# Kernel tuning notes

Hardware: AMD Instinct MI355X
Metric: run time of the kernel (lower is better)

Reference implementation:

```python
import jax, jax.numpy as jnp
import numpy as np

# Config (matches init_kwargs)
S = 8            # num_seqs
LQ = 256         # query tokens per sequence (num_tokens = S*LQ = 2048)
SEQ = 2048       # kv seq_len per sequence
BLK = 16         # block size
NBLK_PER_SEQ = SEQ // BLK   # 128 = max_num_blocks_per_seq
NUM_BLKS = S * NBLK_PER_SEQ # 1024
HQ = 32          # num_query_heads
HKV = 8          # num_kv_heads
G = HQ // HKV    # queries per kv head (GQA group)
D = 128          # head_size
WINDOW = 1024    # sliding_window
SCALE = 1.0 / float(np.sqrt(D))


def setup_inputs() -> dict:
    key = jax.random.key(0)
    k1, k2, k3 = jax.random.split(key, 3)
    query = jax.random.normal(k1, (S * LQ, HQ, D), jnp.float32)
    key_cache = jax.random.normal(k2, (NUM_BLKS, BLK, HKV, D), jnp.float32)
    value_cache = jax.random.normal(k3, (NUM_BLKS, BLK, HKV, D), jnp.float32)
    # each sequence owns a contiguous run of blocks; all indices valid (>=0)
    block_tables = jnp.arange(NUM_BLKS, dtype=jnp.int32).reshape(S, NBLK_PER_SEQ)
    seq_lens = jnp.full((S,), SEQ, dtype=jnp.int32)
    query_start_len = (jnp.arange(S + 1, dtype=jnp.int32) * LQ)
    return dict(query=query, key_cache=key_cache, value_cache=value_cache,
                block_tables=block_tables, seq_lens=seq_lens,
                query_start_len=query_start_len)


def reference(query, key_cache, value_cache, block_tables, seq_lens, query_start_len):
    # query: [S*LQ, HQ, D] -> [S, LQ, HKV, G, D]
    q = query.reshape(S, LQ, HKV, G, D)
    # paged KV gather: [S, NBLK_PER_SEQ] -> [S, NBLK_PER_SEQ, BLK, HKV, D] -> [S, SEQ, HKV, D]
    K = key_cache[block_tables].reshape(S, SEQ, HKV, D)
    V = value_cache[block_tables].reshape(S, SEQ, HKV, D)
    # attention scores: [S, HKV, G, LQ, SEQ]
    scores = jnp.einsum('sqhgd,skhd->shgqk', q, K) * SCALE
    # causal + sliding-window mask over absolute positions
    ctx = SEQ - LQ  # context_len (same for all seqs here)
    qpos = ctx + jnp.arange(LQ)          # [LQ] absolute query positions
    kpos = jnp.arange(SEQ)               # [SEQ] absolute key positions
    valid = (kpos[None, :] <= qpos[:, None]) & \
            (qpos[:, None] - kpos[None, :] < WINDOW)   # [LQ, SEQ]
    neg_inf = jnp.asarray(-jnp.inf, scores.dtype)
    scores = jnp.where(valid[None, None, None, :, :], scores, neg_inf)
    probs = jax.nn.softmax(scores, axis=-1)
    # output: [S, LQ, HKV, G, D] -> [S*LQ, HQ, D]
    out = jnp.einsum('shgqk,skhd->sqhgd', probs, V)
    return out.reshape(S * LQ, HQ, D)
```

## Files before the change

kernel.cpp:

```cpp
#include <hip/hip_runtime.h>
#include <stdint.h>

typedef __attribute__((ext_vector_type(8))) short short8;
typedef __attribute__((ext_vector_type(4))) float floatx4;
typedef __attribute__((ext_vector_type(16))) float f32x16;
typedef __attribute__((ext_vector_type(4))) unsigned int uint4v;
typedef __attribute__((ext_vector_type(2))) unsigned int uint2v;

#define NSEQ 8
#define BLKSZ 16
#define NBLK_PER_SEQ 128
#define HQN 32
#define HKVN 8
#define GQ 4
#define HD 128
#define WINDOW 1024
#define QSCALE 0.12751744f

#define QB 32
#define KVB 64
#define KROW 136
#define VROW 72

#define MFMA32 __builtin_amdgcn_mfma_f32_32x32x16_bf16

static __device__ __forceinline__ unsigned int pack2bf(float lo, float hi) {
    unsigned int a = __builtin_bit_cast(unsigned int, lo) + 0x8000u;
    unsigned int b = __builtin_bit_cast(unsigned int, hi) + 0x8000u;
    return __builtin_amdgcn_perm(b, a, 0x07060302u);
}

static __device__ __forceinline__ float xhalf_max(float x) {
    return fmaxf(x, __shfl_xor(x, 32));
}

extern __shared__ char smem[];

__global__ __launch_bounds__(256, 2)
void attn_fwd(const float* __restrict__ qg,
              const float* __restrict__ kg,
              const float* __restrict__ vg,
              const int* __restrict__ bt,
              const int* __restrict__ seqlens,
              const int* __restrict__ qsl,
              float* __restrict__ outg)
{
    short (*Klds)[KVB][KROW] = (short(*)[KVB][KROW])smem;
    short (*Vt)[HD][VROW]    = (short(*)[HD][VROW])(smem + 34816);

    const int tid  = threadIdx.x;
    const int lane = tid & 63;
    const int wave = tid >> 6;
    const int l31  = lane & 31;
    const int hi   = lane >> 5;

    const int b  = blockIdx.x;
    const int h  = b & 7;
    const int qt = (b >> 3) & 7;
    const int s  = b >> 6;
    const int q0 = qt * QB;

    const int qstart = qsl[s];
    const int numq   = qsl[s + 1] - qstart;
    const int slen   = seqlens[s];
    const int ctx    = slen - numq;
    const int hq     = h * GQ + wave;

    short8 qf[8];
    {
        const float* qrow = qg + ((size_t)(qstart + q0 + l31) * HQN + hq) * HD;
        #pragma unroll
        for (int ks = 0; ks < 8; ++ks) {
            floatx4 f0 = *(const floatx4*)(qrow + ks * 16 + hi * 8);
            floatx4 f1 = *(const floatx4*)(qrow + ks * 16 + hi * 8 + 4);
            uint4v w;
            w[0] = pack2bf(f0[0] * QSCALE, f0[1] * QSCALE);
            w[1] = pack2bf(f0[2] * QSCALE, f0[3] * QSCALE);
            w[2] = pack2bf(f1[0] * QSCALE, f1[1] * QSCALE);
            w[3] = pack2bf(f1[2] * QSCALE, f1[3] * QSCALE);
            qf[ks] = __builtin_bit_cast(short8, w);
        }
    }

    f32x16 oacc[4];
    #pragma unroll
    for (int dblk = 0; dblk < 4; ++dblk)
        #pragma unroll
        for (int i = 0; i < 16; ++i)
            oacc[dblk][i] = 0.f;

    float mrun = -INFINITY;
    float lrun = 0.f;

    int lo = ctx + q0 - WINDOW + 1; if (lo < 0) lo = 0;
    int hiq = ctx + q0 + QB - 1;    if (hiq > slen - 1) hiq = slen - 1;
    const int t0 = lo / KVB, t1 = hiq / KVB;

    const int srow = tid >> 3;
    const int sd0  = (tid & 7) * 16;
    const int j4   = tid & 15;
    const int d0v  = (tid >> 4) * 8;

    floatx4 fk[8], fv[8];

#define LOAD_K_HALF(kv0_, p) {                                                       \
        const int kvp = (kv0_) + (p) * 32 + srow;                                    \
        const int blk = bt[s * NBLK_PER_SEQ + (kvp >> 4)];                           \
        const float* src = kg + (((size_t)blk * BLKSZ + (kvp & 15)) * HKVN + h) * HD + sd0; \
        fk[(p)*4+0] = *(const floatx4*)(src);                                        \
        fk[(p)*4+1] = *(const floatx4*)(src + 4);                                    \
        fk[(p)*4+2] = *(const floatx4*)(src + 8);                                    \
        fk[(p)*4+3] = *(const floatx4*)(src + 12);                                   \
    }
#define LOAD_V(kv0_) {                                                               \
        const int kvv = (kv0_) + 4 * j4;                                             \
        const int blkv = bt[s * NBLK_PER_SEQ + (kvv >> 4)];                          \
        const float* vsrc = vg + (((size_t)blkv * BLKSZ + (kvv & 15)) * HKVN + h) * HD + d0v; \
        fv[0] = *(const floatx4*)(vsrc);                                             \
        fv[4] = *(const floatx4*)(vsrc + 4);                                         \
        fv[1] = *(const floatx4*)(vsrc + 1024);                                      \
        fv[5] = *(const floatx4*)(vsrc + 1028);                                      \
        fv[2] = *(const floatx4*)(vsrc + 2048);                                      \
        fv[6] = *(const floatx4*)(vsrc + 2052);                                      \
        fv[3] = *(const floatx4*)(vsrc + 3072);                                      \
        fv[7] = *(const floatx4*)(vsrc + 3076);                                      \
    }
#define LOAD_TILE(kv0_) { LOAD_K_HALF(kv0_, 0); LOAD_K_HALF(kv0_, 1); LOAD_V(kv0_); }

    LOAD_TILE(t0 * KVB);

    for (int t = t0; t <= t1; ++t) {
        const int kv0 = t * KVB;
        const int vb  = t & 1;

        #pragma unroll
        for (int p = 0; p < 2; ++p) {
            const int row = p * 32 + srow;
            uint4v w;
            w[0] = pack2bf(fk[p*4+0][0], fk[p*4+0][1]);
            w[1] = pack2bf(fk[p*4+0][2], fk[p*4+0][3]);
            w[2] = pack2bf(fk[p*4+1][0], fk[p*4+1][1]);
            w[3] = pack2bf(fk[p*4+1][2], fk[p*4+1][3]);
            *(uint4v*)&Klds[vb][row][sd0] = w;
            w[0] = pack2bf(fk[p*4+2][0], fk[p*4+2][1]);
            w[1] = pack2bf(fk[p*4+2][2], fk[p*4+2][3]);
            w[2] = pack2bf(fk[p*4+3][0], fk[p*4+3][1]);
            w[3] = pack2bf(fk[p*4+3][2], fk[p*4+3][3]);
            *(uint4v*)&Klds[vb][row][sd0 + 8] = w;
        }
        #pragma unroll
        for (int d = 0; d < 8; ++d) {
            const float r0 = (d < 4) ? fv[0][d] : fv[4][d - 4];
            const float r1 = (d < 4) ? fv[1][d] : fv[5][d - 4];
            const float r2 = (d < 4) ? fv[2][d] : fv[6][d - 4];
            const float r3 = (d < 4) ? fv[3][d] : fv[7][d - 4];
            uint2v w;
            w[0] = pack2bf(r0, r1);
            w[1] = pack2bf(r2, r3);
            *(uint2v*)&Vt[vb][d0v + d][4 * j4] = w;
        }

        __syncthreads();

        f32x16 sacc0, sacc1;
        #pragma unroll
        for (int i = 0; i < 16; ++i) { sacc0[i] = 0.f; sacc1[i] = 0.f; }
        #pragma unroll
        for (int ks = 0; ks < 8; ++ks) {
            short8 kf0 = *(const short8*)&Klds[vb][l31][ks * 16 + hi * 8];
            short8 kf1 = *(const short8*)&Klds[vb][32 + l31][ks * 16 + hi * 8];
            sacc0 = MFMA32(kf0, qf[ks], sacc0, 0, 0, 0);
            sacc1 = MFMA32(kf1, qf[ks], sacc1, 0, 0, 0);
        }

        if (t < t1) LOAD_TILE(kv0 + KVB);

        const bool interior = (kv0 >= ctx + q0 - (WINDOW - QB)) &&
                              (kv0 + KVB - 1 <= ctx + q0);
        const int qpos = ctx + q0 + l31;
        float p2[2][16];
        #pragma unroll
        for (int m2 = 0; m2 < 2; ++m2) {
            #pragma unroll
            for (int r = 0; r < 16; ++r) {
                float x = (m2 == 0) ? sacc0[r] : sacc1[r];
                if (!interior) {
                    const int kpos = kv0 + m2 * 32 + (r & 3) + 4 * hi + 8 * (r >> 2);
                    const bool valid = (kpos <= qpos) && (qpos - kpos < WINDOW);
                    x = valid ? x : -INFINITY;
                }
                p2[m2][r] = x;
            }
        }
        float tmax[16];
        #pragma unroll
        for (int r = 0; r < 16; ++r) tmax[r] = fmaxf(p2[0][r], p2[1][r]);
        #pragma unroll
        for (int s2 = 8; s2 > 0; s2 >>= 1)
            #pragma unroll
            for (int r = 0; r < 8; ++r)
                if (r < s2) tmax[r] = fmaxf(tmax[r], tmax[r + s2]);
        float rmax = xhalf_max(tmax[0]);

        const float mold = mrun;
        const bool defer = __all(rmax <= mold + 11.0f);
        const float mnew = defer ? mold : fmaxf(mold, rmax);
        const float alpha = defer ? 1.0f
            : ((mold == -INFINITY) ? ((mnew == -INFINITY) ? 1.0f : 0.0f)
                                   : exp2f(mold - mnew));
        const bool dead = (mnew == -INFINITY);
        #pragma unroll
        for (int m2 = 0; m2 < 2; ++m2)
            #pragma unroll
            for (int r = 0; r < 16; ++r)
                p2[m2][r] = dead ? 0.f : exp2f(p2[m2][r] - mnew);
        float ts[16];
        #pragma unroll
        for (int r = 0; r < 16; ++r) ts[r] = p2[0][r] + p2[1][r];
        #pragma unroll
        for (int s2 = 8; s2 > 0; s2 >>= 1)
            #pragma unroll
            for (int r = 0; r < 8; ++r)
                if (r < s2) ts[r] = ts[r] + ts[r + s2];
        lrun = lrun * alpha + ts[0];
        mrun = mnew;
        if (!defer) {
            #pragma unroll
            for (int dblk = 0; dblk < 4; ++dblk)
                oacc[dblk] = oacc[dblk] * alpha;
        }

        short8 pb[2][2];
        #pragma unroll
        for (int m2 = 0; m2 < 2; ++m2) {
            unsigned int c0 = pack2bf(p2[m2][0],  p2[m2][1]);
            unsigned int c1 = pack2bf(p2[m2][2],  p2[m2][3]);
            unsigned int c2 = pack2bf(p2[m2][4],  p2[m2][5]);
            unsigned int c3 = pack2bf(p2[m2][6],  p2[m2][7]);
            unsigned int c4 = pack2bf(p2[m2][8],  p2[m2][9]);
            unsigned int c5 = pack2bf(p2[m2][10], p2[m2][11]);
            unsigned int c6 = pack2bf(p2[m2][12], p2[m2][13]);
            unsigned int c7 = pack2bf(p2[m2][14], p2[m2][15]);
            unsigned int s0 = hi ? c0 : c2;
            unsigned int s1 = hi ? c1 : c3;
            unsigned int s2 = hi ? c4 : c6;
            unsigned int s3 = hi ? c5 : c7;
            unsigned int r0 = (unsigned int)__shfl_xor((int)s0, 32);
            unsigned int r1 = (unsigned int)__shfl_xor((int)s1, 32);
            unsigned int r2 = (unsigned int)__shfl_xor((int)s2, 32);
            unsigned int r3 = (unsigned int)__shfl_xor((int)s3, 32);
            uint4v u0, u1;
            u0[0] = hi ? r0 : c0;
            u0[1] = hi ? r1 : c1;
            u0[2] = hi ? c2 : r0;
            u0[3] = hi ? c3 : r1;
            u1[0] = hi ? r2 : c4;
            u1[1] = hi ? r3 : c5;
            u1[2] = hi ? c6 : r2;
            u1[3] = hi ? c7 : r3;
            pb[m2][0] = __builtin_bit_cast(short8, u0);
            pb[m2][1] = __builtin_bit_cast(short8, u1);
        }

        #pragma unroll
        for (int m2 = 0; m2 < 2; ++m2) {
            #pragma unroll
            for (int dblk = 0; dblk < 4; ++dblk) {
                short8 vf0 = *(const short8*)&Vt[vb][dblk * 32 + l31][m2 * 32 + hi * 8];
                short8 vf1 = *(const short8*)&Vt[vb][dblk * 32 + l31][m2 * 32 + 16 + hi * 8];
                oacc[dblk] = MFMA32(vf0, pb[m2][0], oacc[dblk], 0, 0, 0);
                oacc[dblk] = MFMA32(vf1, pb[m2][1], oacc[dblk], 0, 0, 0);
            }
        }
    }
#undef LOAD_TILE
#undef LOAD_V
#undef LOAD_K_HALF

    {
        const float ltot = lrun + __shfl_xor(lrun, 32);
        const float inv = 1.0f / ltot;
        float* orow = outg + ((size_t)(qstart + q0 + l31) * HQN + hq) * HD;
        #pragma unroll
        for (int dblk = 0; dblk < 4; ++dblk) {
            #pragma unroll
            for (int rq = 0; rq < 4; ++rq) {
                floatx4 o;
                o[0] = oacc[dblk][4 * rq + 0] * inv;
                o[1] = oacc[dblk][4 * rq + 1] * inv;
                o[2] = oacc[dblk][4 * rq + 2] * inv;
                o[3] = oacc[dblk][4 * rq + 3] * inv;
                *(floatx4*)(orow + dblk * 32 + 8 * rq + 4 * hi) = o;
            }
        }
    }
}

extern "C" void kernel_launch(void* const* d_in, const int* in_sizes, int n_in,
                              void* d_out, int out_size, void* d_ws, size_t ws_size,
                              hipStream_t stream) {
    const float* q  = (const float*)d_in[0];
    const float* k  = (const float*)d_in[1];
    const float* v  = (const float*)d_in[2];
    const int* btp  = (const int*)d_in[3];
    const int* sl   = (const int*)d_in[4];
    const int* qs   = (const int*)d_in[5];
    float* out      = (float*)d_out;

    hipFuncSetAttribute((const void*)attn_fwd,
                        hipFuncAttributeMaxDynamicSharedMemorySize, 71680);
    attn_fwd<<<dim3(NSEQ * HKVN * 8), 256, 71680, stream>>>(q, k, v, btp, sl, qs, out);
}
```

Baseline: 78.71 us.

## Process two KV tiles per iteration with a single softmax update

```diff
diff --git a/kernel.cpp b/kernel.cpp
--- a/kernel.cpp
+++ b/kernel.cpp
@@ -127,74 +127,100 @@
     }
 #define LOAD_TILE(kv0_) { LOAD_K_HALF(kv0_, 0); LOAD_K_HALF(kv0_, 1); LOAD_V(kv0_); }
 
+#define STORE_TILE(bi) {                                                             \
+        _Pragma("unroll")                                                            \
+        for (int p = 0; p < 2; ++p) {                                                \
+            const int row = p * 32 + srow;                                           \
+            uint4v w;                                                                \
+            w[0] = pack2bf(fk[p*4+0][0], fk[p*4+0][1]);                              \
+            w[1] = pack2bf(fk[p*4+0][2], fk[p*4+0][3]);                              \
+            w[2] = pack2bf(fk[p*4+1][0], fk[p*4+1][1]);                              \
+            w[3] = pack2bf(fk[p*4+1][2], fk[p*4+1][3]);                              \
+            *(uint4v*)&Klds[bi][row][sd0] = w;                                       \
+            w[0] = pack2bf(fk[p*4+2][0], fk[p*4+2][1]);                              \
+            w[1] = pack2bf(fk[p*4+2][2], fk[p*4+2][3]);                              \
+            w[2] = pack2bf(fk[p*4+3][0], fk[p*4+3][1]);                              \
+            w[3] = pack2bf(fk[p*4+3][2], fk[p*4+3][3]);                              \
+            *(uint4v*)&Klds[bi][row][sd0 + 8] = w;                                   \
+        }                                                                            \
+        _Pragma("unroll")                                                            \
+        for (int d = 0; d < 8; ++d) {                                                \
+            const float r0 = (d < 4) ? fv[0][d] : fv[4][d - 4];                      \
+            const float r1 = (d < 4) ? fv[1][d] : fv[5][d - 4];                      \
+            const float r2 = (d < 4) ? fv[2][d] : fv[6][d - 4];                      \
+            const float r3 = (d < 4) ? fv[3][d] : fv[7][d - 4];                      \
+            uint2v w2;                                                               \
+            w2[0] = pack2bf(r0, r1);                                                 \
+            w2[1] = pack2bf(r2, r3);                                                 \
+            *(uint2v*)&Vt[bi][d0v + d][4 * j4] = w2;                                 \
+        }                                                                            \
+    }
+
     LOAD_TILE(t0 * KVB);
 
-    for (int t = t0; t <= t1; ++t) {
-        const int kv0 = t * KVB;
-        const int vb  = t & 1;
-
-        #pragma unroll
-        for (int p = 0; p < 2; ++p) {
-            const int row = p * 32 + srow;
-            uint4v w;
-            w[0] = pack2bf(fk[p*4+0][0], fk[p*4+0][1]);
-            w[1] = pack2bf(fk[p*4+0][2], fk[p*4+0][3]);
-            w[2] = pack2bf(fk[p*4+1][0], fk[p*4+1][1]);
-            w[3] = pack2bf(fk[p*4+1][2], fk[p*4+1][3]);
-            *(uint4v*)&Klds[vb][row][sd0] = w;
-            w[0] = pack2bf(fk[p*4+2][0], fk[p*4+2][1]);
-            w[1] = pack2bf(fk[p*4+2][2], fk[p*4+2][3]);
-            w[2] = pack2bf(fk[p*4+3][0], fk[p*4+3][1]);
-            w[3] = pack2bf(fk[p*4+3][2], fk[p*4+3][3]);
-            *(uint4v*)&Klds[vb][row][sd0 + 8] = w;
-        }
-        #pragma unroll
-        for (int d = 0; d < 8; ++d) {
-            const float r0 = (d < 4) ? fv[0][d] : fv[4][d - 4];
-            const float r1 = (d < 4) ? fv[1][d] : fv[5][d - 4];
-            const float r2 = (d < 4) ? fv[2][d] : fv[6][d - 4];
-            const float r3 = (d < 4) ? fv[3][d] : fv[7][d - 4];
-            uint2v w;
-            w[0] = pack2bf(r0, r1);
-            w[1] = pack2bf(r2, r3);
-            *(uint2v*)&Vt[vb][d0v + d][4 * j4] = w;
-        }
+    for (int t = t0; t <= t1; t += 2) {
+        const int kv0A = t * KVB;
+        const int kv0B = kv0A + KVB;
+        const bool hasB = (t + 1 <= t1);
+
+        STORE_TILE(0);
 
         __syncthreads();
 
-        f32x16 sacc0, sacc1;
-        #pragma unroll
-        for (int i = 0; i < 16; ++i) { sacc0[i] = 0.f; sacc1[i] = 0.f; }
+        if (hasB) LOAD_TILE(kv0B);
+
+        f32x16 saccA0, saccA1;
+        #pragma unroll
+        for (int i = 0; i < 16; ++i) { saccA0[i] = 0.f; saccA1[i] = 0.f; }
         #pragma unroll
         for (int ks = 0; ks < 8; ++ks) {
-            short8 kf0 = *(const short8*)&Klds[vb][l31][ks * 16 + hi * 8];
-            short8 kf1 = *(const short8*)&Klds[vb][32 + l31][ks * 16 + hi * 8];
-            sacc0 = MFMA32(kf0, qf[ks], sacc0, 0, 0, 0);
-            sacc1 = MFMA32(kf1, qf[ks], sacc1, 0, 0, 0);
-        }
-
-        if (t < t1) LOAD_TILE(kv0 + KVB);
-
-        const bool interior = (kv0 >= ctx + q0 - (WINDOW - QB)) &&
-                              (kv0 + KVB - 1 <= ctx + q0);
+            short8 kf0 = *(const short8*)&Klds[0][l31][ks * 16 + hi * 8];
+            short8 kf1 = *(const short8*)&Klds[0][32 + l31][ks * 16 + hi * 8];
+            saccA0 = MFMA32(kf0, qf[ks], saccA0, 0, 0, 0);
+            saccA1 = MFMA32(kf1, qf[ks], saccA1, 0, 0, 0);
+        }
+
+        if (hasB) STORE_TILE(1);
+
+        __syncthreads();
+
+        f32x16 saccB0, saccB1;
+        #pragma unroll
+        for (int i = 0; i < 16; ++i) { saccB0[i] = 0.f; saccB1[i] = 0.f; }
+        if (hasB) {
+            #pragma unroll
+            for (int ks = 0; ks < 8; ++ks) {
+                short8 kf0 = *(const short8*)&Klds[1][l31][ks * 16 + hi * 8];
+                short8 kf1 = *(const short8*)&Klds[1][32 + l31][ks * 16 + hi * 8];
+                saccB0 = MFMA32(kf0, qf[ks], saccB0, 0, 0, 0);
+                saccB1 = MFMA32(kf1, qf[ks], saccB1, 0, 0, 0);
+            }
+        }
+
         const int qpos = ctx + q0 + l31;
-        float p2[2][16];
-        #pragma unroll
-        for (int m2 = 0; m2 < 2; ++m2) {
+        float p2[4][16];
+        #pragma unroll
+        for (int m4 = 0; m4 < 4; ++m4) {
+            const int kv0h = kv0A + m4 * 32;
+            const bool live = (m4 < 2) || hasB;
+            const bool interior = live &&
+                (kv0h >= ctx + q0 - (WINDOW - QB)) && (kv0h + 31 <= ctx + q0);
             #pragma unroll
             for (int r = 0; r < 16; ++r) {
-                float x = (m2 == 0) ? sacc0[r] : sacc1[r];
+                float x = (m4 == 0) ? saccA0[r] : (m4 == 1) ? saccA1[r]
+                        : (m4 == 2) ? saccB0[r] : saccB1[r];
                 if (!interior) {
-                    const int kpos = kv0 + m2 * 32 + (r & 3) + 4 * hi + 8 * (r >> 2);
-                    const bool valid = (kpos <= qpos) && (qpos - kpos < WINDOW);
+                    const int kpos = kv0h + (r & 3) + 4 * hi + 8 * (r >> 2);
+                    const bool valid = live && (kpos <= qpos) && (qpos - kpos < WINDOW);
                     x = valid ? x : -INFINITY;
                 }
-                p2[m2][r] = x;
+                p2[m4][r] = x;
             }
         }
         float tmax[16];
         #pragma unroll
-        for (int r = 0; r < 16; ++r) tmax[r] = fmaxf(p2[0][r], p2[1][r]);
+        for (int r = 0; r < 16; ++r)
+            tmax[r] = fmaxf(fmaxf(p2[0][r], p2[1][r]), fmaxf(p2[2][r], p2[3][r]));
         #pragma unroll
         for (int s2 = 8; s2 > 0; s2 >>= 1)
             #pragma unroll
@@ -210,13 +236,14 @@
                                    : exp2f(mold - mnew));
         const bool dead = (mnew == -INFINITY);
         #pragma unroll
-        for (int m2 = 0; m2 < 2; ++m2)
+        for (int m4 = 0; m4 < 4; ++m4)
             #pragma unroll
             for (int r = 0; r < 16; ++r)
-                p2[m2][r] = dead ? 0.f : exp2f(p2[m2][r] - mnew);
+                p2[m4][r] = dead ? 0.f : exp2f(p2[m4][r] - mnew);
         float ts[16];
         #pragma unroll
-        for (int r = 0; r < 16; ++r) ts[r] = p2[0][r] + p2[1][r];
+        for (int r = 0; r < 16; ++r)
+            ts[r] = (p2[0][r] + p2[1][r]) + (p2[2][r] + p2[3][r]);
         #pragma unroll
         for (int s2 = 8; s2 > 0; s2 >>= 1)
             #pragma unroll
@@ -230,17 +257,17 @@
                 oacc[dblk] = oacc[dblk] * alpha;
         }
 
-        short8 pb[2][2];
-        #pragma unroll
-        for (int m2 = 0; m2 < 2; ++m2) {
-            unsigned int c0 = pack2bf(p2[m2][0],  p2[m2][1]);
-            unsigned int c1 = pack2bf(p2[m2][2],  p2[m2][3]);
-            unsigned int c2 = pack2bf(p2[m2][4],  p2[m2][5]);
-            unsigned int c3 = pack2bf(p2[m2][6],  p2[m2][7]);
-            unsigned int c4 = pack2bf(p2[m2][8],  p2[m2][9]);
-            unsigned int c5 = pack2bf(p2[m2][10], p2[m2][11]);
-            unsigned int c6 = pack2bf(p2[m2][12], p2[m2][13]);
-            unsigned int c7 = pack2bf(p2[m2][14], p2[m2][15]);
+        short8 pb[4][2];
+        #pragma unroll
+        for (int m4 = 0; m4 < 4; ++m4) {
+            unsigned int c0 = pack2bf(p2[m4][0],  p2[m4][1]);
+            unsigned int c1 = pack2bf(p2[m4][2],  p2[m4][3]);
+            unsigned int c2 = pack2bf(p2[m4][4],  p2[m4][5]);
+            unsigned int c3 = pack2bf(p2[m4][6],  p2[m4][7]);
+            unsigned int c4 = pack2bf(p2[m4][8],  p2[m4][9]);
+            unsigned int c5 = pack2bf(p2[m4][10], p2[m4][11]);
+            unsigned int c6 = pack2bf(p2[m4][12], p2[m4][13]);
+            unsigned int c7 = pack2bf(p2[m4][14], p2[m4][15]);
             unsigned int s0 = hi ? c0 : c2;
             unsigned int s1 = hi ? c1 : c3;
             unsigned int s2 = hi ? c4 : c6;
@@ -258,21 +285,38 @@
             u1[1] = hi ? r3 : c5;
             u1[2] = hi ? c6 : r2;
             u1[3] = hi ? c7 : r3;
-            pb[m2][0] = __builtin_bit_cast(short8, u0);
-            pb[m2][1] = __builtin_bit_cast(short8, u1);
-        }
+            pb[m4][0] = __builtin_bit_cast(short8, u0);
+            pb[m4][1] = __builtin_bit_cast(short8, u1);
+        }
+
+        if (t + 2 <= t1) LOAD_TILE(kv0A + 2 * KVB);
 
         #pragma unroll
         for (int m2 = 0; m2 < 2; ++m2) {
             #pragma unroll
             for (int dblk = 0; dblk < 4; ++dblk) {
-                short8 vf0 = *(const short8*)&Vt[vb][dblk * 32 + l31][m2 * 32 + hi * 8];
-                short8 vf1 = *(const short8*)&Vt[vb][dblk * 32 + l31][m2 * 32 + 16 + hi * 8];
+                short8 vf0 = *(const short8*)&Vt[0][dblk * 32 + l31][m2 * 32 + hi * 8];
+                short8 vf1 = *(const short8*)&Vt[0][dblk * 32 + l31][m2 * 32 + 16 + hi * 8];
                 oacc[dblk] = MFMA32(vf0, pb[m2][0], oacc[dblk], 0, 0, 0);
                 oacc[dblk] = MFMA32(vf1, pb[m2][1], oacc[dblk], 0, 0, 0);
             }
         }
-    }
+        if (hasB) {
+            #pragma unroll
+            for (int m2 = 0; m2 < 2; ++m2) {
+                #pragma unroll
+                for (int dblk = 0; dblk < 4; ++dblk) {
+                    short8 vf0 = *(const short8*)&Vt[1][dblk * 32 + l31][m2 * 32 + hi * 8];
+                    short8 vf1 = *(const short8*)&Vt[1][dblk * 32 + l31][m2 * 32 + 16 + hi * 8];
+                    oacc[dblk] = MFMA32(vf0, pb[2 + m2][0], oacc[dblk], 0, 0, 0);
+                    oacc[dblk] = MFMA32(vf1, pb[2 + m2][1], oacc[dblk], 0, 0, 0);
+                }
+            }
+        }
+
+        __syncthreads();
+    }
+#undef STORE_TILE
 #undef LOAD_TILE
 #undef LOAD_V
 #undef LOAD_K_HALF
```

After: 166.3 us. 111% more time.
